# Performance work log

Hardware: AMD Instinct MI355X
Metric: run time of the kernel (lower is better)

## Reference

```python
import jax, jax.numpy as jnp
import numpy as np

BS, D, C, L_MAP, N_LAYERS, IMG = 8, 512, 128, 8, 9, 64


def _leaky(x):
    return jnp.where(x >= 0, x, 0.2 * x)


def _conv2d_mod(x, style, weight):
    # x: [bs, C, H, W], style: [bs, C], weight: [Cout, Cin, 3, 3]
    # modulate along input-channel dim, demodulate per (sample, out-channel)
    mw = weight[None] * style[:, None, :, None, None]          # [bs, Cout, Cin, 3, 3]
    rstd = jax.lax.rsqrt(jnp.sum(mw * mw, axis=(2, 3, 4), keepdims=True) + 1e-8)
    dw = mw * rstd                                             # demodulated per-sample weights

    def per_sample(xi, wi):
        return jax.lax.conv_general_dilated(
            xi[None], wi, window_strides=(1, 1), padding='SAME',
            dimension_numbers=('NCHW', 'OIHW', 'NCHW'))[0]

    return jax.vmap(per_sample)(x, dw)                         # [bs, C, H, W]


def _upsample2x(x):
    b, c, h, w = x.shape
    return jax.image.resize(x, (b, c, 2 * h, 2 * w), method='bilinear')


def setup_inputs():
    key = jax.random.key(0)
    ks = jax.random.split(key, 10)
    # kaiming fan_in gain for leaky_relu(a=0) per nn.init in Conv2dMod
    conv_std = float(np.sqrt(2.0 / (C * 9)))
    return {
        'latent_z': jax.random.normal(ks[0], (BS, D), jnp.float32),
        'noise': jax.random.normal(ks[1], (N_LAYERS, BS, IMG * IMG), jnp.float32),
        'map_w': jax.random.normal(ks[2], (L_MAP, D, D), jnp.float32) / np.sqrt(D),
        'map_b': jnp.zeros((L_MAP, D), jnp.float32),
        'A_w': jax.random.normal(ks[3], (N_LAYERS, D, C), jnp.float32) / np.sqrt(D),
        'A_b': jax.random.normal(ks[4], (N_LAYERS, C), jnp.float32) * 0.02 + 1.0,
        'B_w': jax.random.normal(ks[5], (N_LAYERS, C), jnp.float32),
        'B_b': jax.random.normal(ks[6], (N_LAYERS, C), jnp.float32) * 0.02,
        'conv_w': jax.random.normal(ks[7], (N_LAYERS, C, C, 3, 3), jnp.float32) * conv_std,
        'rgb_w': jax.random.normal(ks[8], (3, C, 3, 3), jnp.float32) / np.sqrt(C * 9),
        'rgb_b': jnp.zeros((3,), jnp.float32),
    }


def reference(latent_z, noise, map_w, map_b, A_w, A_b, B_w, B_b, conv_w, rgb_w, rgb_b):
    # ---- Mapping: PixelNorm + n_map_layers FC+LeakyReLU ----
    w = latent_z * jax.lax.rsqrt(jnp.mean(latent_z * latent_z, axis=1, keepdims=True) + 1e-8)
    for i in range(L_MAP):
        w = _leaky(w @ map_w[i] + map_b[i])                    # [bs, D] (same w for every style layer)

    # ---- Synthesis ----
    x = jnp.zeros((BS, C, 4, 4), latent_z.dtype)
    for i in range(N_LAYERS):
        if i % 2 == 1:
            x = _upsample2x(x)
        b, c, h, wd = x.shape
        ns = h * wd
        style = w @ A_w[i] + A_b[i]                            # [bs, C]
        # B: Linear(1, C) on per-pixel noise scalar -> per-channel noise map
        nmap = noise[i][:, :ns, None] * B_w[i][None, None, :] + B_b[i]  # [bs, ns, C]
        nmap = jnp.transpose(nmap, (0, 2, 1)).reshape(b, C, h, wd)
        x = _leaky(_conv2d_mod(x, style, conv_w[i]) + nmap)

    # ---- to RGB ----
    rgb = jax.lax.conv_general_dilated(
        x, rgb_w, window_strides=(1, 1), padding='SAME',
        dimension_numbers=('NCHW', 'OIHW', 'NCHW')) + rgb_b[None, :, None, None]
    return rgb
```

## Files before the change

### kernel.cpp

```cpp
#include <hip/hip_runtime.h>
#include <hip/hip_bf16.h>

#define BS 8
#define D 512
#define CCH 128
#define LMAP 8
#define NLAYERS 9

typedef short short8 __attribute__((ext_vector_type(8)));
typedef short short4v __attribute__((ext_vector_type(4)));
typedef float f32x4 __attribute__((ext_vector_type(4)));

__device__ short g_bufA[(size_t)BS * 4096 * CCH];
__device__ short g_bufB[(size_t)BS * 4096 * CCH];
__device__ float g_w[2][BS * D];
__device__ float g_style_all[NLAYERS * BS * CCH];
__device__ float g_rstd_all[NLAYERS * BS * CCH];
__device__ short g_wpack[(size_t)NLAYERS * 9 * 4 * 8 * 64 * 8];
__device__ short g_rgbpack[9 * 4 * 64 * 8];

__device__ __forceinline__ float leaky(float v) { return v >= 0.f ? v : 0.2f * v; }
__device__ __forceinline__ short f2b(float f) {
    __hip_bfloat16 h = __float2bfloat16(f);
    return *reinterpret_cast<short*>(&h);
}
__device__ __forceinline__ float b2f(short s) {
    return __uint_as_float(((unsigned int)(unsigned short)s) << 16);
}
__device__ __forceinline__ int swz(int col) { return ((col ^ (col >> 3)) & 7) << 3; }

__global__ __launch_bounds__(256) void wprep_kernel(const float* __restrict__ convw)
{
    int idx = blockIdx.x * 256 + threadIdx.x;
    if (idx >= NLAYERS * 9 * 4 * 8 * 64) return;
    int lane = idx & 63;
    int cogrp = (idx >> 6) & 7;
    int chunk = (idx >> 9) & 3;
    int t = idx >> 11;
    int layer = t / 9, tap = t - layer * 9;
    int co = cogrp * 16 + (lane & 15);
    int ci0 = chunk * 32 + (lane >> 4) * 8;
    short8 v;
#pragma unroll
    for (int j = 0; j < 8; ++j)
        v[j] = f2b(convw[(((size_t)layer * CCH + co) * CCH + ci0 + j) * 9 + tap]);
    *reinterpret_cast<short8*>(&g_wpack[(size_t)idx * 8]) = v;
}

__global__ void rgbprep_kernel(const float* __restrict__ rgbw)
{
    int idx = blockIdx.x * 256 + threadIdx.x;
    if (idx >= 9 * 4 * 64) return;
    int lane = idx & 63;
    int chunk = (idx >> 6) & 3;
    int tap = idx >> 8;
    int co = lane & 15;
    int ci0 = chunk * 32 + (lane >> 4) * 8;
    short8 v;
#pragma unroll
    for (int j = 0; j < 8; ++j)
        v[j] = (co < 3) ? f2b(rgbw[((size_t)(co * CCH) + ci0 + j) * 9 + tap]) : (short)0;
    *reinterpret_cast<short8*>(&g_rgbpack[(size_t)idx * 8]) = v;
}

__global__ __launch_bounds__(256) void map_fc_kernel(
    int srcSel, int useZ, const float* __restrict__ z,
    const float* __restrict__ W, const float* __restrict__ bias)
{
    float* wout = g_w[srcSel ^ 1];
    int b = blockIdx.y;
    int jb = blockIdx.x * 64;
    int tid = threadIdx.x;
    int jl = tid & 63, kp = tid >> 6;
    __shared__ float xin[D];
    __shared__ float part[4][64];
    __shared__ float wred[4];
    if (useZ) {
        xin[tid] = z[b * D + tid];
        xin[tid + 256] = z[b * D + tid + 256];
    } else {
        const float* win = g_w[srcSel];
        xin[tid] = win[b * D + tid];
        xin[tid + 256] = win[b * D + tid + 256];
    }
    __syncthreads();
    if (useZ) {
        float p = xin[tid] * xin[tid] + xin[tid + 256] * xin[tid + 256];
#pragma unroll
        for (int off = 32; off > 0; off >>= 1) p += __shfl_down(p, off, 64);
        if ((tid & 63) == 0) wred[tid >> 6] = p;
        __syncthreads();
        float ss = wred[0] + wred[1] + wred[2] + wred[3];
        float r = rsqrtf(ss * (1.f / 512.f) + 1e-8f);
        xin[tid] *= r; xin[tid + 256] *= r;
        __syncthreads();
    }
    const float* Wp = W + jb + jl;
    const int k0 = kp * 128;
    float a0 = 0.f, a1 = 0.f, a2 = 0.f, a3 = 0.f, a4 = 0.f, a5 = 0.f, a6 = 0.f, a7 = 0.f;
    for (int k = k0; k < k0 + 128; k += 8) {
        a0 += xin[k + 0] * Wp[(size_t)(k + 0) * D];
        a1 += xin[k + 1] * Wp[(size_t)(k + 1) * D];
        a2 += xin[k + 2] * Wp[(size_t)(k + 2) * D];
        a3 += xin[k + 3] * Wp[(size_t)(k + 3) * D];
        a4 += xin[k + 4] * Wp[(size_t)(k + 4) * D];
        a5 += xin[k + 5] * Wp[(size_t)(k + 5) * D];
        a6 += xin[k + 6] * Wp[(size_t)(k + 6) * D];
        a7 += xin[k + 7] * Wp[(size_t)(k + 7) * D];
    }
    part[kp][jl] = ((a0 + a1) + (a2 + a3)) + ((a4 + a5) + (a6 + a7));
    __syncthreads();
    if (tid < 64) {
        float s = part[0][tid] + part[1][tid] + part[2][tid] + part[3][tid] + bias[jb + tid];
        wout[b * D + jb + tid] = leaky(s);
    }
}

__global__ __launch_bounds__(256) void style_rstd_kernel(
    const float* __restrict__ Aw, const float* __restrict__ Ab,
    const float* __restrict__ convw)
{
    int l = blockIdx.x + 1;
    int b = blockIdx.y;
    int tid = threadIdx.x;
    __shared__ float ws_[D];
    __shared__ float part[2][CCH];
    __shared__ float st[CCH];
    ws_[tid] = g_w[0][b * D + tid];
    ws_[tid + 256] = g_w[0][b * D + tid + 256];
    __syncthreads();
    {
        int c = tid & 127, kh = tid >> 7;
        const float* Ap = Aw + (size_t)l * D * CCH + c;
        const int k0 = kh * 256;
        float a0 = 0.f, a1 = 0.f, a2 = 0.f, a3 = 0.f, a4 = 0.f, a5 = 0.f, a6 = 0.f, a7 = 0.f;
        for (int k = k0; k < k0 + 256; k += 8) {
            a0 += ws_[k + 0] * Ap[(size_t)(k + 0) * CCH];
            a1 += ws_[k + 1] * Ap[(size_t)(k + 1) * CCH];
            a2 += ws_[k + 2] * Ap[(size_t)(k + 2) * CCH];
            a3 += ws_[k + 3] * Ap[(size_t)(k + 3) * CCH];
            a4 += ws_[k + 4] * Ap[(size_t)(k + 4) * CCH];
            a5 += ws_[k + 5] * Ap[(size_t)(k + 5) * CCH];
            a6 += ws_[k + 6] * Ap[(size_t)(k + 6) * CCH];
            a7 += ws_[k + 7] * Ap[(size_t)(k + 7) * CCH];
        }
        part[kh][c] = ((a0 + a1) + (a2 + a3)) + ((a4 + a5) + (a6 + a7));
    }
    __syncthreads();
    if (tid < CCH) {
        float s = part[0][tid] + part[1][tid] + Ab[l * CCH + tid];
        st[tid] = s;
        g_style_all[((size_t)l * BS + b) * CCH + tid] = s;
    }
    __syncthreads();
    int colid = tid >> 4, kpart = tid & 15;
    for (int co8 = 0; co8 < 8; ++co8) {
        int cout = co8 * 16 + colid;
        const float* wp = convw + ((size_t)(l * CCH + cout) * CCH + kpart * 8) * 9;
        float wf[72];
#pragma unroll
        for (int q = 0; q < 18; ++q) {
            float4 t = *reinterpret_cast<const float4*>(wp + q * 4);
            wf[q * 4 + 0] = t.x; wf[q * 4 + 1] = t.y; wf[q * 4 + 2] = t.z; wf[q * 4 + 3] = t.w;
        }
        float s = 0.f;
#pragma unroll
        for (int ci = 0; ci < 8; ++ci) {
            float sv = st[kpart * 8 + ci];
#pragma unroll
            for (int k = 0; k < 9; ++k) { float m = wf[ci * 9 + k] * sv; s += m * m; }
        }
#pragma unroll
        for (int off = 8; off > 0; off >>= 1) s += __shfl_down(s, off, 16);
        if (kpart == 0) g_rstd_all[((size_t)l * BS + b) * CCH + cout] = rsqrtf(s + 1e-8f);
    }
}

__global__ void layer0_kernel(const float* __restrict__ noise,
                              const float* __restrict__ Bw, const float* __restrict__ Bb)
{
    int idx = blockIdx.x * 256 + threadIdx.x;
    if (idx >= BS * 16 * CCH) return;
    int c = idx & 127;
    int pix = (idx >> 7) & 15;
    int b = idx >> 11;
    float v = leaky(noise[b * 4096 + pix] * Bw[c] + Bb[c]);
    v *= g_style_all[((size_t)1 * BS + b) * CCH + c];
    g_bufA[((size_t)b * 16 + pix) * CCH + c] = f2b(v);
}

__global__ void upsample_kernel(int srcSel, int LWin)
{
    const short* in = srcSel ? g_bufB : g_bufA;
    short* out = srcSel ? g_bufA : g_bufB;
    const int Win = 1 << LWin, Wo = Win * 2;
    const int total = BS * Wo * Wo * 16;
    int idx = blockIdx.x * 256 + threadIdx.x;
    if (idx >= total) return;
    int ck = idx & 15;
    int x = (idx >> 4) & (Wo - 1);
    int y = (idx >> (4 + LWin + 1)) & (Wo - 1);
    int b = idx >> (4 + 2 * (LWin + 1));
    int my = y >> 1, mx = x >> 1;
    int y0, y1, x0, x1;
    float wy0, wy1, wx0, wx1;
    if ((y & 1) == 0) { y0 = my - 1; y1 = my; wy0 = 0.25f; wy1 = 0.75f; if (y0 < 0) { y0 = 0; wy0 = 0.f; wy1 = 1.f; } }
    else              { y0 = my; y1 = my + 1; wy0 = 0.75f; wy1 = 0.25f; if (y1 >= Win) { y1 = Win - 1; wy0 = 1.f; wy1 = 0.f; } }
    if ((x & 1) == 0) { x0 = mx - 1; x1 = mx; wx0 = 0.25f; wx1 = 0.75f; if (x0 < 0) { x0 = 0; wx0 = 0.f; wx1 = 1.f; } }
    else              { x0 = mx; x1 = mx + 1; wx0 = 0.75f; wx1 = 0.25f; if (x1 >= Win) { x1 = Win - 1; wx0 = 1.f; wx1 = 0.f; } }
    const short* base = in + (size_t)b * Win * Win * CCH + ck * 8;
    short8 a00 = *reinterpret_cast<const short8*>(&base[(size_t)(y0 * Win + x0) * CCH]);
    short8 a01 = *reinterpret_cast<const short8*>(&base[(size_t)(y0 * Win + x1) * CCH]);
    short8 a10 = *reinterpret_cast<const short8*>(&base[(size_t)(y1 * Win + x0) * CCH]);
    short8 a11 = *reinterpret_cast<const short8*>(&base[(size_t)(y1 * Win + x1) * CCH]);
    short8 o;
#pragma unroll
    for (int j = 0; j < 8; ++j) {
        float v = wy0 * (wx0 * b2f(a00[j]) + wx1 * b2f(a01[j]))
                + wy1 * (wx0 * b2f(a10[j]) + wx1 * b2f(a11[j]));
        o[j] = f2b(v);
    }
    *reinterpret_cast<short8*>(&out[((size_t)b * Wo * Wo + y * Wo + x) * CCH + ck * 8]) = o;
}

template<int LW>
__global__ __launch_bounds__(256) void conv_mfma_kernel(
    int srcSel, int layer, int layerNext,
    const float* __restrict__ noise,
    const float* __restrict__ Bw, const float* __restrict__ Bb)
{
    constexpr int W = 1 << LW;
    constexpr int R = 64 >> LW;
    constexpr int SW = W + 2;
    constexpr int ROWS = R + 2;
    constexpr int NS = W * W;

    const short* xin = srcSel ? g_bufB : g_bufA;
    short* xout = srcSel ? g_bufA : g_bufB;

    const int b = blockIdx.y;
    const int pixBase = blockIdx.x * 64;
    const int rowBase = pixBase >> LW;
    const int tid = threadIdx.x;
    const int lane = tid & 63;
    const int wave = tid >> 6;

    __shared__ short xs[ROWS * SW * CCH];
    __shared__ float style_s[CCH];

    if (tid < CCH)
        style_s[tid] = layerNext ? g_style_all[((size_t)layerNext * BS + b) * CCH + tid] : 1.f;

    {
        const short* src = xin + (size_t)b * NS * CCH;
        constexpr int UN = ROWS * SW * 16;
        for (int u = tid; u < UN; u += 256) {
            int ck = u & 15;
            int rem = u >> 4;
            int col = rem % SW;
            int rr = rem / SW;
            int gy = rowBase + rr - 1, gx = col - 1;
            short8 v = {0, 0, 0, 0, 0, 0, 0, 0};
            if (gy >= 0 && gy < W && gx >= 0 && gx < W)
                v = *reinterpret_cast<const short8*>(&src[((size_t)gy * W + gx) * CCH + ck * 8]);
            *reinterpret_cast<short8*>(&xs[(((rr * SW + col) * CCH) + ck * 8) ^ swz(col)]) = v;
        }
    }
    __syncthreads();

    int rL[4], cL[4];
#pragma unroll
    for (int pf = 0; pf < 4; ++pf) {
        int pl = pf * 16 + (lane & 15);
        cL[pf] = pl & (W - 1);
        rL[pf] = pl >> LW;
    }
    const int grpoff = (lane >> 4) * 8;

    f32x4 acc[2][4] = {};
    const short* wl0 = g_wpack + ((size_t)layer * 9 * 4 * 8 * 64
                                  + (size_t)(wave * 2) * 64 + lane) * 8;
    const short* wl1 = wl0 + 64 * 8;

    short8 wc0 = *reinterpret_cast<const short8*>(wl0);
    short8 wc1 = *reinterpret_cast<const short8*>(wl1);
#pragma unroll
    for (int k = 0; k < 36; ++k) {
        short8 wn0 = wc0, wn1 = wc1;
        if (k + 1 < 36) {
            wn0 = *reinterpret_cast<const short8*>(wl0 + (size_t)(k + 1) * 4096);
            wn1 = *reinterpret_cast<const short8*>(wl1 + (size_t)(k + 1) * 4096);
        }
        const int tap = k >> 2, ch = k & 3;
        const int ky = tap / 3, kx = tap - ky * 3;
#pragma unroll
        for (int pf = 0; pf < 4; ++pf) {
            int col = cL[pf] + kx;
            int idx = (((rL[pf] + ky) * SW + col) * CCH + (ch << 5) + grpoff) ^ swz(col);
            short8 xf = *reinterpret_cast<const short8*>(&xs[idx]);
            acc[0][pf] = __builtin_amdgcn_mfma_f32_16x16x32_bf16(wc0, xf, acc[0][pf], 0, 0, 0);
            acc[1][pf] = __builtin_amdgcn_mfma_f32_16x16x32_bf16(wc1, xf, acc[1][pf], 0, 0, 0);
        }
        wc0 = wn0; wc1 = wn1;
    }

    float nz[4];
#pragma unroll
    for (int pf = 0; pf < 4; ++pf)
        nz[pf] = noise[b * 4096 + pixBase + pf * 16 + (lane & 15)];
#pragma unroll
    for (int cf = 0; cf < 2; ++cf) {
        const int coB = (wave * 2 + cf) * 16 + (lane >> 4) * 4;
        float rs[4], bw[4], bb[4], sn[4];
#pragma unroll
        for (int r = 0; r < 4; ++r) {
            rs[r] = g_rstd_all[((size_t)layer * BS + b) * CCH + coB + r];
            bw[r] = Bw[coB + r];
            bb[r] = Bb[coB + r];
            sn[r] = style_s[coB + r];
        }
#pragma unroll
        for (int pf = 0; pf < 4; ++pf) {
            int px = pixBase + pf * 16 + (lane & 15);
            short4v o;
#pragma unroll
            for (int r = 0; r < 4; ++r) {
                float v = leaky(acc[cf][pf][r] * rs[r] + nz[pf] * bw[r] + bb[r]) * sn[r];
                o[r] = f2b(v);
            }
            *reinterpret_cast<short4v*>(&xout[((size_t)b * NS + px) * CCH + coB]) = o;
        }
    }
}

__global__ __launch_bounds__(256) void rgb_mfma_kernel(
    int srcSel, const float* __restrict__ rgbb, float* __restrict__ out)
{
    constexpr int W = 64, SW = 66, ROWS = 3, NS = 4096;
    const short* xin = srcSel ? g_bufB : g_bufA;

    const int b = blockIdx.y;
    const int pixBase = blockIdx.x * 64;
    const int rowBase = pixBase >> 6;
    const int tid = threadIdx.x;
    const int lane = tid & 63;
    const int wave = tid >> 6;

    __shared__ short xs[ROWS * SW * CCH];

    {
        const short* src = xin + (size_t)b * NS * CCH;
        constexpr int UN = ROWS * SW * 16;
        for (int u = tid; u < UN; u += 256) {
            int ck = u & 15;
            int rem = u >> 4;
            int col = rem % SW;
            int rr = rem / SW;
            int gy = rowBase + rr - 1, gx = col - 1;
            short8 v = {0, 0, 0, 0, 0, 0, 0, 0};
            if (gy >= 0 && gy < W && gx >= 0 && gx < W)
                v = *reinterpret_cast<const short8*>(&src[((size_t)gy * W + gx) * CCH + ck * 8]);
            *reinterpret_cast<short8*>(&xs[(((rr * SW + col) * CCH) + ck * 8) ^ swz(col)]) = v;
        }
    }
    __syncthreads();

    const int grpoff = (lane >> 4) * 8;
    const int cl = lane & 15;
    f32x4 acc[4] = {};
#pragma unroll
    for (int tap = 0; tap < 9; ++tap) {
        const int ky = tap / 3, kx = tap - ky * 3;
        short8 wf = *reinterpret_cast<const short8*>(
            &g_rgbpack[((size_t)(tap * 4 + wave) * 64 + lane) * 8]);
#pragma unroll
        for (int pf = 0; pf < 4; ++pf) {
            int col = cl + pf * 16 + kx;
            int idx = ((ky * SW + col) * CCH + (wave << 5) + grpoff) ^ swz(col);
            short8 xf = *reinterpret_cast<const short8*>(&xs[idx]);
            acc[pf] = __builtin_amdgcn_mfma_f32_16x16x32_bf16(wf, xf, acc[pf], 0, 0, 0);
        }
    }
    __syncthreads();
    float* red = reinterpret_cast<float*>(xs);
    if (wave > 0) {
#pragma unroll
        for (int pf = 0; pf < 4; ++pf)
#pragma unroll
            for (int r = 0; r < 4; ++r)
                red[(((wave - 1) * 4 + pf) * 64 + lane) * 4 + r] = acc[pf][r];
    }
    __syncthreads();
    if (wave == 0 && (lane >> 4) == 0) {
#pragma unroll
        for (int pf = 0; pf < 4; ++pf) {
            int px = pixBase + pf * 16 + cl;
#pragma unroll
            for (int r = 0; r < 3; ++r) {
                float s = acc[pf][r];
#pragma unroll
                for (int wv = 0; wv < 3; ++wv)
                    s += red[((wv * 4 + pf) * 64 + lane) * 4 + r];
                out[(size_t)(b * 3 + r) * NS + px] = s + rgbb[r];
            }
        }
    }
}

extern "C" void kernel_launch(void* const* d_in, const int* in_sizes, int n_in,
                              void* d_out, int out_size, void* d_ws, size_t ws_size,
                              hipStream_t stream)
{
    const float* latent = (const float*)d_in[0];
    const float* noise  = (const float*)d_in[1];
    const float* map_w  = (const float*)d_in[2];
    const float* map_b  = (const float*)d_in[3];
    const float* A_w    = (const float*)d_in[4];
    const float* A_b    = (const float*)d_in[5];
    const float* B_w    = (const float*)d_in[6];
    const float* B_b    = (const float*)d_in[7];
    const float* conv_w = (const float*)d_in[8];
    const float* rgb_w  = (const float*)d_in[9];
    const float* rgb_b  = (const float*)d_in[10];
    float* out = (float*)d_out;
    (void)d_ws; (void)ws_size;

    wprep_kernel<<<(NLAYERS * 9 * 4 * 8 * 64 + 255) / 256, 256, 0, stream>>>(conv_w);
    rgbprep_kernel<<<(9 * 4 * 64 + 255) / 256, 256, 0, stream>>>(rgb_w);

    int wsel = 0;
    for (int i = 0; i < LMAP; ++i) {
        map_fc_kernel<<<dim3(8, BS), 256, 0, stream>>>(
            wsel, i == 0 ? 1 : 0, latent, map_w + (size_t)i * D * D, map_b + i * D);
        wsel ^= 1;
    }

    style_rstd_kernel<<<dim3(8, BS), 256, 0, stream>>>(A_w, A_b, conv_w);

    layer0_kernel<<<(BS * 16 * CCH + 255) / 256, 256, 0, stream>>>(noise, B_w, B_b);

    int cur = 0;
    int Hc = 4;
    for (int i = 1; i < NLAYERS; ++i) {
        if (i & 1) {
            int lwin = (Hc == 4) ? 2 : (Hc == 8) ? 3 : (Hc == 16) ? 4 : 5;
            int total = BS * (Hc * 2) * (Hc * 2) * 16;
            upsample_kernel<<<(total + 255) / 256, 256, 0, stream>>>(cur, lwin);
            Hc *= 2;
            cur ^= 1;
        }
        int ns = Hc * Hc;
        int lnext = (i < 8) ? (i + 1) : 0;
        dim3 grid(ns / 64, BS);
        const float* nz = noise + (size_t)i * BS * 4096;
        switch (Hc) {
            case 8:  conv_mfma_kernel<3><<<grid, 256, 0, stream>>>(cur, i, lnext, nz, B_w + i * CCH, B_b + i * CCH); break;
            case 16: conv_mfma_kernel<4><<<grid, 256, 0, stream>>>(cur, i, lnext, nz, B_w + i * CCH, B_b + i * CCH); break;
            case 32: conv_mfma_kernel<5><<<grid, 256, 0, stream>>>(cur, i, lnext, nz, B_w + i * CCH, B_b + i * CCH); break;
            case 64: conv_mfma_kernel<6><<<grid, 256, 0, stream>>>(cur, i, lnext, nz, B_w + i * CCH, B_b + i * CCH); break;
        }
        cur ^= 1;
    }

    rgb_mfma_kernel<<<dim3(64, BS), 256, 0, stream>>>(cur, rgb_b, out);
}
```

Baseline: 225.8 us.

## Fuse upsample and layer0 into conv loads, collapse mapping MLP into one kernel

New measurement: 315.9 us. +39.9%, slower.

```diff
diff --git a/kernel.cpp b/kernel.cpp
--- a/kernel.cpp
+++ b/kernel.cpp
@@ -13,7 +13,7 @@
 
 __device__ short g_bufA[(size_t)BS * 4096 * CCH];
 __device__ short g_bufB[(size_t)BS * 4096 * CCH];
-__device__ float g_w[2][BS * D];
+__device__ float g_w[BS * D];
 __device__ float g_style_all[NLAYERS * BS * CCH];
 __device__ float g_rstd_all[NLAYERS * BS * CCH];
 __device__ short g_wpack[(size_t)NLAYERS * 9 * 4 * 8 * 64 * 8];
@@ -28,6 +28,13 @@
     return __uint_as_float(((unsigned int)(unsigned short)s) << 16);
 }
 __device__ __forceinline__ int swz(int col) { return ((col ^ (col >> 3)) & 7) << 3; }
+
+__device__ __forceinline__ void uptaps(int o, int Win, int& i0, int& i1, float& w0, float& w1)
+{
+    int m = o >> 1;
+    if ((o & 1) == 0) { i0 = m - 1; i1 = m; w0 = 0.25f; w1 = 0.75f; if (i0 < 0) { i0 = 0; w0 = 0.f; w1 = 1.f; } }
+    else              { i0 = m; i1 = m + 1; w0 = 0.75f; w1 = 0.25f; if (i1 >= Win) { i1 = Win - 1; w0 = 1.f; w1 = 0.f; } }
+}
 
 __global__ __launch_bounds__(256) void wprep_kernel(const float* __restrict__ convw)
 {
@@ -63,57 +70,50 @@
     *reinterpret_cast<short8*>(&g_rgbpack[(size_t)idx * 8]) = v;
 }
 
-__global__ __launch_bounds__(256) void map_fc_kernel(
-    int srcSel, int useZ, const float* __restrict__ z,
-    const float* __restrict__ W, const float* __restrict__ bias)
-{
-    float* wout = g_w[srcSel ^ 1];
-    int b = blockIdx.y;
-    int jb = blockIdx.x * 64;
-    int tid = threadIdx.x;
-    int jl = tid & 63, kp = tid >> 6;
-    __shared__ float xin[D];
-    __shared__ float part[4][64];
+__global__ __launch_bounds__(256) void map_all_kernel(
+    const float* __restrict__ z, const float* __restrict__ Wall, const float* __restrict__ ball)
+{
+    const int b = blockIdx.x;
+    const int tid = threadIdx.x;
+    __shared__ float wbuf[2][D];
     __shared__ float wred[4];
-    if (useZ) {
-        xin[tid] = z[b * D + tid];
-        xin[tid + 256] = z[b * D + tid + 256];
-    } else {
-        const float* win = g_w[srcSel];
-        xin[tid] = win[b * D + tid];
-        xin[tid + 256] = win[b * D + tid + 256];
-    }
-    __syncthreads();
-    if (useZ) {
-        float p = xin[tid] * xin[tid] + xin[tid + 256] * xin[tid + 256];
-#pragma unroll
-        for (int off = 32; off > 0; off >>= 1) p += __shfl_down(p, off, 64);
-        if ((tid & 63) == 0) wred[tid >> 6] = p;
+
+    float v0 = z[b * D + tid], v1 = z[b * D + tid + 256];
+    float p = v0 * v0 + v1 * v1;
+#pragma unroll
+    for (int off = 32; off > 0; off >>= 1) p += __shfl_down(p, off, 64);
+    if ((tid & 63) == 0) wred[tid >> 6] = p;
+    __syncthreads();
+    float ss = wred[0] + wred[1] + wred[2] + wred[3];
+    float r = rsqrtf(ss * (1.f / 512.f) + 1e-8f);
+    wbuf[0][tid] = v0 * r;
+    wbuf[0][tid + 256] = v1 * r;
+    __syncthreads();
+
+    for (int l = 0; l < LMAP; ++l) {
+        const float* src = wbuf[l & 1];
+        float* dst = wbuf[(l & 1) ^ 1];
+        const float* Wc = Wall + (size_t)l * D * D + tid;
+        float a0 = 0.f, a1 = 0.f, a2 = 0.f, a3 = 0.f;
+        float c0 = 0.f, c1 = 0.f, c2 = 0.f, c3 = 0.f;
+        for (int k = 0; k < D; k += 4) {
+            float x0 = src[k], x1 = src[k + 1], x2 = src[k + 2], x3 = src[k + 3];
+            a0 += x0 * Wc[(size_t)(k + 0) * D];
+            a1 += x1 * Wc[(size_t)(k + 1) * D];
+            a2 += x2 * Wc[(size_t)(k + 2) * D];
+            a3 += x3 * Wc[(size_t)(k + 3) * D];
+            c0 += x0 * Wc[(size_t)(k + 0) * D + 256];
+            c1 += x1 * Wc[(size_t)(k + 1) * D + 256];
+            c2 += x2 * Wc[(size_t)(k + 2) * D + 256];
+            c3 += x3 * Wc[(size_t)(k + 3) * D + 256];
+        }
         __syncthreads();
-        float ss = wred[0] + wred[1] + wred[2] + wred[3];
-        float r = rsqrtf(ss * (1.f / 512.f) + 1e-8f);
-        xin[tid] *= r; xin[tid + 256] *= r;
+        dst[tid] = leaky((a0 + a1) + (a2 + a3) + ball[l * D + tid]);
+        dst[tid + 256] = leaky((c0 + c1) + (c2 + c3) + ball[l * D + tid + 256]);
         __syncthreads();
     }
-    const float* Wp = W + jb + jl;
-    const int k0 = kp * 128;
-    float a0 = 0.f, a1 = 0.f, a2 = 0.f, a3 = 0.f, a4 = 0.f, a5 = 0.f, a6 = 0.f, a7 = 0.f;
-    for (int k = k0; k < k0 + 128; k += 8) {
-        a0 += xin[k + 0] * Wp[(size_t)(k + 0) * D];
-        a1 += xin[k + 1] * Wp[(size_t)(k + 1) * D];
-        a2 += xin[k + 2] * Wp[(size_t)(k + 2) * D];
-        a3 += xin[k + 3] * Wp[(size_t)(k + 3) * D];
-        a4 += xin[k + 4] * Wp[(size_t)(k + 4) * D];
-        a5 += xin[k + 5] * Wp[(size_t)(k + 5) * D];
-        a6 += xin[k + 6] * Wp[(size_t)(k + 6) * D];
-        a7 += xin[k + 7] * Wp[(size_t)(k + 7) * D];
-    }
-    part[kp][jl] = ((a0 + a1) + (a2 + a3)) + ((a4 + a5) + (a6 + a7));
-    __syncthreads();
-    if (tid < 64) {
-        float s = part[0][tid] + part[1][tid] + part[2][tid] + part[3][tid] + bias[jb + tid];
-        wout[b * D + jb + tid] = leaky(s);
-    }
+    g_w[b * D + tid] = wbuf[0][tid];
+    g_w[b * D + tid + 256] = wbuf[0][tid + 256];
 }
 
 __global__ __launch_bounds__(256) void style_rstd_kernel(
@@ -126,8 +126,8 @@
     __shared__ float ws_[D];
     __shared__ float part[2][CCH];
     __shared__ float st[CCH];
-    ws_[tid] = g_w[0][b * D + tid];
-    ws_[tid + 256] = g_w[0][b * D + tid + 256];
+    ws_[tid] = g_w[b * D + tid];
+    ws_[tid + 256] = g_w[b * D + tid + 256];
     __syncthreads();
     {
         int c = tid & 127, kh = tid >> 7;
@@ -176,64 +176,20 @@
     }
 }
 
-__global__ void layer0_kernel(const float* __restrict__ noise,
-                              const float* __restrict__ Bw, const float* __restrict__ Bb)
-{
-    int idx = blockIdx.x * 256 + threadIdx.x;
-    if (idx >= BS * 16 * CCH) return;
-    int c = idx & 127;
-    int pix = (idx >> 7) & 15;
-    int b = idx >> 11;
-    float v = leaky(noise[b * 4096 + pix] * Bw[c] + Bb[c]);
-    v *= g_style_all[((size_t)1 * BS + b) * CCH + c];
-    g_bufA[((size_t)b * 16 + pix) * CCH + c] = f2b(v);
-}
-
-__global__ void upsample_kernel(int srcSel, int LWin)
-{
-    const short* in = srcSel ? g_bufB : g_bufA;
-    short* out = srcSel ? g_bufA : g_bufB;
-    const int Win = 1 << LWin, Wo = Win * 2;
-    const int total = BS * Wo * Wo * 16;
-    int idx = blockIdx.x * 256 + threadIdx.x;
-    if (idx >= total) return;
-    int ck = idx & 15;
-    int x = (idx >> 4) & (Wo - 1);
-    int y = (idx >> (4 + LWin + 1)) & (Wo - 1);
-    int b = idx >> (4 + 2 * (LWin + 1));
-    int my = y >> 1, mx = x >> 1;
-    int y0, y1, x0, x1;
-    float wy0, wy1, wx0, wx1;
-    if ((y & 1) == 0) { y0 = my - 1; y1 = my; wy0 = 0.25f; wy1 = 0.75f; if (y0 < 0) { y0 = 0; wy0 = 0.f; wy1 = 1.f; } }
-    else              { y0 = my; y1 = my + 1; wy0 = 0.75f; wy1 = 0.25f; if (y1 >= Win) { y1 = Win - 1; wy0 = 1.f; wy1 = 0.f; } }
-    if ((x & 1) == 0) { x0 = mx - 1; x1 = mx; wx0 = 0.25f; wx1 = 0.75f; if (x0 < 0) { x0 = 0; wx0 = 0.f; wx1 = 1.f; } }
-    else              { x0 = mx; x1 = mx + 1; wx0 = 0.75f; wx1 = 0.25f; if (x1 >= Win) { x1 = Win - 1; wx0 = 1.f; wx1 = 0.f; } }
-    const short* base = in + (size_t)b * Win * Win * CCH + ck * 8;
-    short8 a00 = *reinterpret_cast<const short8*>(&base[(size_t)(y0 * Win + x0) * CCH]);
-    short8 a01 = *reinterpret_cast<const short8*>(&base[(size_t)(y0 * Win + x1) * CCH]);
-    short8 a10 = *reinterpret_cast<const short8*>(&base[(size_t)(y1 * Win + x0) * CCH]);
-    short8 a11 = *reinterpret_cast<const short8*>(&base[(size_t)(y1 * Win + x1) * CCH]);
-    short8 o;
-#pragma unroll
-    for (int j = 0; j < 8; ++j) {
-        float v = wy0 * (wx0 * b2f(a00[j]) + wx1 * b2f(a01[j]))
-                + wy1 * (wx0 * b2f(a10[j]) + wx1 * b2f(a11[j]));
-        o[j] = f2b(v);
-    }
-    *reinterpret_cast<short8*>(&out[((size_t)b * Wo * Wo + y * Wo + x) * CCH + ck * 8]) = o;
-}
-
-template<int LW>
+template<int LW, int UPM>
 __global__ __launch_bounds__(256) void conv_mfma_kernel(
     int srcSel, int layer, int layerNext,
     const float* __restrict__ noise,
-    const float* __restrict__ Bw, const float* __restrict__ Bb)
+    const float* __restrict__ Bw, const float* __restrict__ Bb,
+    const float* __restrict__ noise0,
+    const float* __restrict__ Bw0, const float* __restrict__ Bb0)
 {
     constexpr int W = 1 << LW;
     constexpr int R = 64 >> LW;
     constexpr int SW = W + 2;
     constexpr int ROWS = R + 2;
     constexpr int NS = W * W;
+    constexpr int WIN = W / 2;
 
     const short* xin = srcSel ? g_bufB : g_bufA;
     short* xout = srcSel ? g_bufA : g_bufB;
@@ -247,9 +203,137 @@
 
     __shared__ short xs[ROWS * SW * CCH];
     __shared__ float style_s[CCH];
+    constexpr int SMSZ = (UPM == 2) ? 16 * CCH : 1;
+    __shared__ short sm[SMSZ];
 
     if (tid < CCH)
         style_s[tid] = layerNext ? g_style_all[((size_t)layerNext * BS + b) * CCH + tid] : 1.f;
+
+    if (UPM == 2) {
+        for (int u = tid; u < 16 * CCH; u += 256) {
+            int c = u & 127;
+            int pp = u >> 7;
+            float v = leaky(noise0[b * 4096 + pp] * Bw0[c] + Bb0[c])
+                      * g_style_all[((size_t)1 * BS + b) * CCH + c];
+            sm[u] = f2b(v);
+        }
+        __syncthreads();
+    }
+
+    {
+        const short* src = xin + (size_t)b * NS * CCH;
+        const short* srcH = xin + (size_t)b * WIN * WIN * CCH;
+        constexpr int UN = ROWS * SW * 16;
+        for (int u = tid; u < UN; u += 256) {
+            int ck = u & 15;
+            int rem = u >> 4;
+            int col = rem % SW;
+            int rr = rem / SW;
+            int gy = rowBase + rr - 1, gx = col - 1;
+            short8 v = {0, 0, 0, 0, 0, 0, 0, 0};
+            if (gy >= 0 && gy < W && gx >= 0 && gx < W) {
+                if (UPM == 0) {
+                    v = *reinterpret_cast<const short8*>(&src[((size_t)gy * W + gx) * CCH + ck * 8]);
+                } else {
+                    int y0, y1, x0, x1; float wy0, wy1, wx0, wx1;
+                    uptaps(gy, WIN, y0, y1, wy0, wy1);
+                    uptaps(gx, WIN, x0, x1, wx0, wx1);
+                    const short* sp = (UPM == 2) ? sm : srcH;
+                    short8 a00 = *reinterpret_cast<const short8*>(&sp[((size_t)y0 * WIN + x0) * CCH + ck * 8]);
+                    short8 a01 = *reinterpret_cast<const short8*>(&sp[((size_t)y0 * WIN + x1) * CCH + ck * 8]);
+                    short8 a10 = *reinterpret_cast<const short8*>(&sp[((size_t)y1 * WIN + x0) * CCH + ck * 8]);
+                    short8 a11 = *reinterpret_cast<const short8*>(&sp[((size_t)y1 * WIN + x1) * CCH + ck * 8]);
+                    float w00 = wy0 * wx0, w01 = wy0 * wx1, w10 = wy1 * wx0, w11 = wy1 * wx1;
+#pragma unroll
+                    for (int j = 0; j < 8; ++j)
+                        v[j] = f2b(w00 * b2f(a00[j]) + w01 * b2f(a01[j])
+                                 + w10 * b2f(a10[j]) + w11 * b2f(a11[j]));
+                }
+            }
+            *reinterpret_cast<short8*>(&xs[(((rr * SW + col) * CCH) + ck * 8) ^ swz(col)]) = v;
+        }
+    }
+    __syncthreads();
+
+    int rL[4], cL[4];
+#pragma unroll
+    for (int pf = 0; pf < 4; ++pf) {
+        int pl = pf * 16 + (lane & 15);
+        cL[pf] = pl & (W - 1);
+        rL[pf] = pl >> LW;
+    }
+    const int grpoff = (lane >> 4) * 8;
+
+    f32x4 acc[2][4] = {};
+    const short* wl0 = g_wpack + ((size_t)layer * 9 * 4 * 8 * 64
+                                  + (size_t)(wave * 2) * 64 + lane) * 8;
+    const short* wl1 = wl0 + 64 * 8;
+
+    short8 wc0 = *reinterpret_cast<const short8*>(wl0);
+    short8 wc1 = *reinterpret_cast<const short8*>(wl1);
+#pragma unroll
+    for (int k = 0; k < 36; ++k) {
+        short8 wn0 = wc0, wn1 = wc1;
+        if (k + 1 < 36) {
+            wn0 = *reinterpret_cast<const short8*>(wl0 + (size_t)(k + 1) * 4096);
+            wn1 = *reinterpret_cast<const short8*>(wl1 + (size_t)(k + 1) * 4096);
+        }
+        const int tap = k >> 2, ch = k & 3;
+        const int ky = tap / 3, kx = tap - ky * 3;
+#pragma unroll
+        for (int pf = 0; pf < 4; ++pf) {
+            int col = cL[pf] + kx;
+            int idx = (((rL[pf] + ky) * SW + col) * CCH + (ch << 5) + grpoff) ^ swz(col);
+            short8 xf = *reinterpret_cast<const short8*>(&xs[idx]);
+            acc[0][pf] = __builtin_amdgcn_mfma_f32_16x16x32_bf16(wc0, xf, acc[0][pf], 0, 0, 0);
+            acc[1][pf] = __builtin_amdgcn_mfma_f32_16x16x32_bf16(wc1, xf, acc[1][pf], 0, 0, 0);
+        }
+        wc0 = wn0; wc1 = wn1;
+    }
+
+    float nz[4];
+#pragma unroll
+    for (int pf = 0; pf < 4; ++pf)
+        nz[pf] = noise[b * 4096 + pixBase + pf * 16 + (lane & 15)];
+#pragma unroll
+    for (int cf = 0; cf < 2; ++cf) {
+        const int coB = (wave * 2 + cf) * 16 + (lane >> 4) * 4;
+        float rs[4], bw[4], bb[4], sn[4];
+#pragma unroll
+        for (int r = 0; r < 4; ++r) {
+            rs[r] = g_rstd_all[((size_t)layer * BS + b) * CCH + coB + r];
+            bw[r] = Bw[coB + r];
+            bb[r] = Bb[coB + r];
+            sn[r] = style_s[coB + r];
+        }
+#pragma unroll
+        for (int pf = 0; pf < 4; ++pf) {
+            int px = pixBase + pf * 16 + (lane & 15);
+            short4v o;
+#pragma unroll
+            for (int r = 0; r < 4; ++r) {
+                float v = leaky(acc[cf][pf][r] * rs[r] + nz[pf] * bw[r] + bb[r]) * sn[r];
+                o[r] = f2b(v);
+            }
+            *reinterpret_cast<short4v*>(&xout[((size_t)b * NS + px) * CCH + coB]) = o;
+        }
+    }
+}
+
+__global__ __launch_bounds__(256) void rgb_mfma_kernel(
+    int srcSel, const float* __restrict__ rgbb, float* __restrict__ out)
+{
+    constexpr int W = 64, SW = 66, ROWS = 3, NS = 4096;
+    const short* xin = srcSel ? g_bufB : g_bufA;
+
+    const int b = blockIdx.y;
+    const int pixBase = blockIdx.x * 64;
+    const int rowBase = pixBase >> 6;
+    const int tid = threadIdx.x;
+    const int lane = tid & 63;
+    const int wave = tid >> 6;
+
+    __shared__ short xs[ROWS * SW * CCH];
 
     {
         const short* src = xin + (size_t)b * NS * CCH;
@@ -268,103 +352,6 @@
     }
     __syncthreads();
 
-    int rL[4], cL[4];
-#pragma unroll
-    for (int pf = 0; pf < 4; ++pf) {
-        int pl = pf * 16 + (lane & 15);
-        cL[pf] = pl & (W - 1);
-        rL[pf] = pl >> LW;
-    }
-    const int grpoff = (lane >> 4) * 8;
-
-    f32x4 acc[2][4] = {};
-    const short* wl0 = g_wpack + ((size_t)layer * 9 * 4 * 8 * 64
-                                  + (size_t)(wave * 2) * 64 + lane) * 8;
-    const short* wl1 = wl0 + 64 * 8;
-
-    short8 wc0 = *reinterpret_cast<const short8*>(wl0);
-    short8 wc1 = *reinterpret_cast<const short8*>(wl1);
-#pragma unroll
-    for (int k = 0; k < 36; ++k) {
-        short8 wn0 = wc0, wn1 = wc1;
-        if (k + 1 < 36) {
-            wn0 = *reinterpret_cast<const short8*>(wl0 + (size_t)(k + 1) * 4096);
-            wn1 = *reinterpret_cast<const short8*>(wl1 + (size_t)(k + 1) * 4096);
-        }
-        const int tap = k >> 2, ch = k & 3;
-        const int ky = tap / 3, kx = tap - ky * 3;
-#pragma unroll
-        for (int pf = 0; pf < 4; ++pf) {
-            int col = cL[pf] + kx;
-            int idx = (((rL[pf] + ky) * SW + col) * CCH + (ch << 5) + grpoff) ^ swz(col);
-            short8 xf = *reinterpret_cast<const short8*>(&xs[idx]);
-            acc[0][pf] = __builtin_amdgcn_mfma_f32_16x16x32_bf16(wc0, xf, acc[0][pf], 0, 0, 0);
-            acc[1][pf] = __builtin_amdgcn_mfma_f32_16x16x32_bf16(wc1, xf, acc[1][pf], 0, 0, 0);
-        }
-        wc0 = wn0; wc1 = wn1;
-    }
-
-    float nz[4];
-#pragma unroll
-    for (int pf = 0; pf < 4; ++pf)
-        nz[pf] = noise[b * 4096 + pixBase + pf * 16 + (lane & 15)];
-#pragma unroll
-    for (int cf = 0; cf < 2; ++cf) {
-        const int coB = (wave * 2 + cf) * 16 + (lane >> 4) * 4;
-        float rs[4], bw[4], bb[4], sn[4];
-#pragma unroll
-        for (int r = 0; r < 4; ++r) {
-            rs[r] = g_rstd_all[((size_t)layer * BS + b) * CCH + coB + r];
-            bw[r] = Bw[coB + r];
-            bb[r] = Bb[coB + r];
-            sn[r] = style_s[coB + r];
-        }
-#pragma unroll
-        for (int pf = 0; pf < 4; ++pf) {
-            int px = pixBase + pf * 16 + (lane & 15);
-            short4v o;
-#pragma unroll
-            for (int r = 0; r < 4; ++r) {
-                float v = leaky(acc[cf][pf][r] * rs[r] + nz[pf] * bw[r] + bb[r]) * sn[r];
-                o[r] = f2b(v);
-            }
-            *reinterpret_cast<short4v*>(&xout[((size_t)b * NS + px) * CCH + coB]) = o;
-        }
-    }
-}
-
-__global__ __launch_bounds__(256) void rgb_mfma_kernel(
-    int srcSel, const float* __restrict__ rgbb, float* __restrict__ out)
-{
-    constexpr int W = 64, SW = 66, ROWS = 3, NS = 4096;
-    const short* xin = srcSel ? g_bufB : g_bufA;
-
-    const int b = blockIdx.y;
-    const int pixBase = blockIdx.x * 64;
-    const int rowBase = pixBase >> 6;
-    const int tid = threadIdx.x;
-    const int lane = tid & 63;
-    const int wave = tid >> 6;
-
-    __shared__ short xs[ROWS * SW * CCH];
-
-    {
-        const short* src = xin + (size_t)b * NS * CCH;
-        constexpr int UN = ROWS * SW * 16;
-        for (int u = tid; u < UN; u += 256) {
-            int ck = u & 15;
-            int rem = u >> 4;
-            int col = rem % SW;
-            int rr = rem / SW;
-            int gy = rowBase + rr - 1, gx = col - 1;
-            short8 v = {0, 0, 0, 0, 0, 0, 0, 0};
-            if (gy >= 0 && gy < W && gx >= 0 && gx < W)
-                v = *reinterpret_cast<const short8*>(&src[((size_t)gy * W + gx) * CCH + ck * 8]);
-            *reinterpret_cast<short8*>(&xs[(((rr * SW + col) * CCH) + ck * 8) ^ swz(col)]) = v;
-        }
-    }
-    __syncthreads();
-
     const int grpoff = (lane >> 4) * 8;
     const int cl = lane & 15;
     f32x4 acc[4] = {};
@@ -428,36 +415,26 @@
     wprep_kernel<<<(NLAYERS * 9 * 4 * 8 * 64 + 255) / 256, 256, 0, stream>>>(conv_w);
     rgbprep_kernel<<<(9 * 4 * 64 + 255) / 256, 256, 0, stream>>>(rgb_w);
 
-    int wsel = 0;
-    for (int i = 0; i < LMAP; ++i) {
-        map_fc_kernel<<<dim3(8, BS), 256, 0, stream>>>(
-            wsel, i == 0 ? 1 : 0, latent, map_w + (size_t)i * D * D, map_b + i * D);
-        wsel ^= 1;
-    }
-
+    map_all_kernel<<<BS, 256, 0, stream>>>(latent, map_w, map_b);
     style_rstd_kernel<<<dim3(8, BS), 256, 0, stream>>>(A_w, A_b, conv_w);
 
-    layer0_kernel<<<(BS * 16 * CCH + 255) / 256, 256, 0, stream>>>(noise, B_w, B_b);
-
-    int cur = 0;
+    int cur = 1;
     int Hc = 4;
     for (int i = 1; i < NLAYERS; ++i) {
-        if (i & 1) {
-            int lwin = (Hc == 4) ? 2 : (Hc == 8) ? 3 : (Hc == 16) ? 4 : 5;
-            int total = BS * (Hc * 2) * (Hc * 2) * 16;
-            upsample_kernel<<<(total + 255) / 256, 256, 0, stream>>>(cur, lwin);
-            Hc *= 2;
-            cur ^= 1;
-        }
+        if (i & 1) Hc *= 2;
         int ns = Hc * Hc;
         int lnext = (i < 8) ? (i + 1) : 0;
         dim3 grid(ns / 64, BS);
         const float* nz = noise + (size_t)i * BS * 4096;
-        switch (Hc) {
-            case 8:  conv_mfma_kernel<3><<<grid, 256, 0, stream>>>(cur, i, lnext, nz, B_w + i * CCH, B_b + i * CCH); break;
-            case 16: conv_mfma_kernel<4><<<grid, 256, 0, stream>>>(cur, i, lnext, nz, B_w + i * CCH, B_b + i * CCH); break;
-            case 32: conv_mfma_kernel<5><<<grid, 256, 0, stream>>>(cur, i, lnext, nz, B_w + i * CCH, B_b + i * CCH); break;
-            case 64: conv_mfma_kernel<6><<<grid, 256, 0, stream>>>(cur, i, lnext, nz, B_w + i * CCH, B_b + i * CCH); break;
+        switch (i) {
+            case 1: conv_mfma_kernel<3, 2><<<grid, 256, 0, stream>>>(cur, i, lnext, nz, B_w + i * CCH, B_b + i * CCH, noise, B_w, B_b); break;
+            case 2: conv_mfma_kernel<3, 0><<<grid, 256, 0, stream>>>(cur, i, lnext, nz, B_w + i * CCH, B_b + i * CCH, noise, B_w, B_b); break;
+            case 3: conv_mfma_kernel<4, 1><<<grid, 256, 0, stream>>>(cur, i, lnext, nz, B_w + i * CCH, B_b + i * CCH, noise, B_w, B_b); break;
+            case 4: conv_mfma_kernel<4, 0><<<grid, 256, 0, stream>>>(cur, i, lnext, nz, B_w + i * CCH, B_b + i * CCH, noise, B_w, B_b); break;
+            case 5: conv_mfma_kernel<5, 1><<<grid, 256, 0, stream>>>(cur, i, lnext, nz, B_w + i * CCH, B_b + i * CCH, noise, B_w, B_b); break;
+            case 6: conv_mfma_kernel<5, 0><<<grid, 256, 0, stream>>>(cur, i, lnext, nz, B_w + i * CCH, B_b + i * CCH, noise, B_w, B_b); break;
+            case 7: conv_mfma_kernel<6, 1><<<grid, 256, 0, stream>>>(cur, i, lnext, nz, B_w + i * CCH, B_b + i * CCH, noise, B_w, B_b); break;
+            case 8: conv_mfma_kernel<6, 0><<<grid, 256, 0, stream>>>(cur, i, lnext, nz, B_w + i * CCH, B_b + i * CCH, noise, B_w, B_b); break;
         }
         cur ^= 1;
     }
```
